# Kernel tuning notes

Hardware: AMD Instinct MI355X
Metric: run time of the kernel (lower is better)

## Reference

```python
import jax, jax.numpy as jnp
import numpy as np

N_NODES = 100000
N_EDGES = 1600000
D_IN = 128
D_HID = 128
SCALE = 1.8
EPS = 1e-12


def setup_inputs() -> dict:
    key = jax.random.key(0)
    ks = jax.random.split(key, 7)
    x = jax.random.normal(ks[0], (N_NODES, D_IN), dtype=jnp.float32)
    W1 = jax.random.normal(ks[1], (D_HID, D_IN), dtype=jnp.float32) * 0.05
    b1 = jax.random.normal(ks[2], (D_HID,), dtype=jnp.float32) * 0.05
    W2 = jax.random.normal(ks[3], (D_HID, D_HID), dtype=jnp.float32) * 0.05
    b2 = jax.random.normal(ks[4], (D_HID,), dtype=jnp.float32) * 0.05
    src = jax.random.randint(ks[5], (N_EDGES,), 0, N_NODES, dtype=jnp.int64 if jax.config.jax_enable_x64 else jnp.int32)
    dst = jax.random.randint(ks[6], (N_EDGES,), 0, N_NODES, dtype=jnp.int64 if jax.config.jax_enable_x64 else jnp.int32)
    return {"x": x, "W1": W1, "b1": b1, "W2": W2, "b2": b2, "src": src, "dst": dst}


def reference(x, W1, b1, W2, b2, src, dst):
    N = x.shape[0]
    ones = jnp.ones((src.shape[0],), dtype=x.dtype)
    # GraphConv norm='both' degree normalizers (clamped to >=1 as in DGL)
    deg_out = jnp.maximum(jnp.zeros((N,), x.dtype).at[src].add(ones), 1.0)
    deg_in = jnp.maximum(jnp.zeros((N,), x.dtype).at[dst].add(ones), 1.0)
    norm_out = jax.lax.rsqrt(deg_out)[:, None]  # [N,1]
    norm_in = jax.lax.rsqrt(deg_in)[:, None]    # [N,1]

    def layer(h, W, b):
        # torch.nn.Linear: h @ W.T + b
        h = jnp.einsum('nd,kd->nk', h, W) + b
        # F.normalize(h, dim=1) * 1.8
        nrm = jnp.sqrt(jnp.sum(h * h, axis=1, keepdims=True))
        h = h / jnp.maximum(nrm, EPS) * SCALE
        # GraphConv (weight=False, bias=False, norm='both'):
        # D_out^{-1/2} -> sparse aggregate -> D_in^{-1/2}
        h = h * norm_out
        agg = jax.ops.segment_sum(h[src], dst, num_segments=N)
        return agg * norm_in

    h = layer(x, W1, b1)
    h = layer(h, W2, b2)
    return h
```

## Files before the change

### kernel.cpp

```cpp
#include <hip/hip_runtime.h>
#include <cstdint>
#include <cstddef>

#define D 128
#define NSCALE 1.8f
#define NEPS 1e-12f
#define EPB 2048
#define NBPAD 784
#define NLO 512
#define SCAP 9216
#define SRCB 23
#define SRCM 0x7FFFFF

typedef __attribute__((ext_vector_type(8))) short bf16x8;
typedef __attribute__((ext_vector_type(4))) float f32x4;

__device__ __forceinline__ ushort bf16_rtn(float f) {
    uint32_t u = __float_as_uint(f);
    u = u + 0x7FFFu + ((u >> 16) & 1u);
    return (ushort)(u >> 16);
}

__device__ __forceinline__ float blo(uint32_t u) { return __uint_as_float(u << 16); }
__device__ __forceinline__ float bhi(uint32_t u) { return __uint_as_float(u & 0xFFFF0000u); }

__global__ __launch_bounds__(256) void hist_high_kernel(const int* __restrict__ src,
                                                        const int* __restrict__ dst,
                                                        int* __restrict__ Hd,
                                                        int* __restrict__ Hs, int ne) {
    __shared__ int hd[256], hs[256];
    int t = threadIdx.x, b = blockIdx.x;
    hd[t] = 0; hs[t] = 0;
    __syncthreads();
    int base = b * EPB, end = min(ne, base + EPB);
    for (int i = base + t; i < end; i += 256) {
        atomicAdd(&hd[dst[i] >> 9], 1);
        atomicAdd(&hs[src[i] >> 9], 1);
    }
    __syncthreads();
    Hd[t * NBPAD + b] = hd[t];
    Hs[t * NBPAD + b] = hs[t];
}

__global__ __launch_bounds__(256) void scan_cols_kernel(int* __restrict__ Hd,
                                                        int* __restrict__ Hs,
                                                        int* __restrict__ total_d,
                                                        int* __restrict__ total_s, int nbk) {
    __shared__ int s[256];
    int* H = blockIdx.y ? Hs : Hd;
    int* tot = blockIdx.y ? total_s : total_d;
    int v = blockIdx.x, t = threadIdx.x;
    int base = v * NBPAD + 4 * t;
    int a0 = (4 * t + 0 < nbk) ? H[base + 0] : 0;
    int a1 = (4 * t + 1 < nbk) ? H[base + 1] : 0;
    int a2 = (4 * t + 2 < nbk) ? H[base + 2] : 0;
    int a3 = (4 * t + 3 < nbk) ? H[base + 3] : 0;
    int sum = a0 + a1 + a2 + a3;
    s[t] = sum;
    __syncthreads();
    #pragma unroll
    for (int off = 1; off < 256; off <<= 1) {
        int u = (t >= off) ? s[t - off] : 0;
        __syncthreads();
        s[t] += u;
        __syncthreads();
    }
    int excl = s[t] - sum;
    if (4 * t + 0 < nbk) H[base + 0] = excl;
    if (4 * t + 1 < nbk) H[base + 1] = excl + a0;
    if (4 * t + 2 < nbk) H[base + 2] = excl + a0 + a1;
    if (4 * t + 3 < nbk) H[base + 3] = excl + a0 + a1 + a2;
    if (t == 255) tot[v] = s[255];
}

__global__ __launch_bounds__(256) void scan_tot_kernel(const int* __restrict__ total_d,
                                                       const int* __restrict__ total_s,
                                                       int* __restrict__ Bd,
                                                       int* __restrict__ Bs, int hb) {
    __shared__ int s[256];
    const int* tot = blockIdx.x ? total_s : total_d;
    int* B = blockIdx.x ? Bs : Bd;
    int t = threadIdx.x;
    int val = (t < hb) ? tot[t] : 0;
    s[t] = val;
    __syncthreads();
    #pragma unroll
    for (int off = 1; off < 256; off <<= 1) {
        int u = (t >= off) ? s[t - off] : 0;
        __syncthreads();
        s[t] += u;
        __syncthreads();
    }
    if (t <= hb) B[t] = s[t] - val;
}

__global__ __launch_bounds__(256) void scatter_high_kernel(const int* __restrict__ src,
                                                           const int* __restrict__ dst,
                                                           const int* __restrict__ Hd,
                                                           const int* __restrict__ Hs,
                                                           const int* __restrict__ Bd,
                                                           const int* __restrict__ Bs,
                                                           uint32_t* __restrict__ spack,
                                                           ushort* __restrict__ ss_low,
                                                           int ne, int hb) {
    __shared__ int cur[256];
    int t = threadIdx.x, b = blockIdx.x;
    int base = b * EPB, end = min(ne, base + EPB);
    if (blockIdx.y == 0) {
        if (t < hb) cur[t] = Bd[t] + Hd[t * NBPAD + b];
        __syncthreads();
        for (int i = base + t; i < end; i += 256) {
            int d = dst[i], s = src[i];
            int pd = atomicAdd(&cur[d >> 9], 1);
            spack[pd] = ((uint32_t)(d & (NLO - 1)) << SRCB) | (uint32_t)s;
        }
    } else {
        if (t < hb) cur[t] = Bs[t] + Hs[t * NBPAD + b];
        __syncthreads();
        for (int i = base + t; i < end; i += 256) {
            int s = src[i];
            int ps = atomicAdd(&cur[s >> 9], 1);
            ss_low[ps] = (ushort)(s & (NLO - 1));
        }
    }
}

__global__ __launch_bounds__(1024) void bucket_sorthist_kernel(const uint32_t* __restrict__ spack,
                                                               const int* __restrict__ Bd,
                                                               const ushort* __restrict__ ss_low,
                                                               const int* __restrict__ Bs,
                                                               int* __restrict__ offs,
                                                               int* __restrict__ cnt_dst,
                                                               float* __restrict__ norm_in,
                                                               float* __restrict__ norm_out,
                                                               int* __restrict__ ssrc, int N) {
    __shared__ int h[NLO], sc[NLO], cur[NLO];
    __shared__ int inA[SCAP];
    __shared__ int stage[SCAP];
    int t = threadIdx.x, v = blockIdx.x;

    if (blockIdx.y == 1) {
        int beg = Bs[v], end = Bs[v + 1];
        if (t < NLO) h[t] = 0;
        __syncthreads();
        for (int i = beg + t; i < end; i += 1024) atomicAdd(&h[(int)ss_low[i]], 1);
        __syncthreads();
        int g = (v << 9) + t;
        if (t < NLO && g < N) norm_out[g] = rsqrtf((float)max(h[t], 1));
        return;
    }

    int beg = Bd[v], end = Bd[v + 1];
    int m = end - beg;
    bool staged = (m <= SCAP);

    if (t < NLO) h[t] = 0;
    if (staged) {
        __syncthreads();
        for (int i = beg + t; i < end; i += 1024) inA[i - beg] = (int)spack[i];
        __syncthreads();
        for (int i = t; i < m; i += 1024) atomicAdd(&h[((uint32_t)inA[i]) >> SRCB], 1);
    } else {
        __syncthreads();
        for (int i = beg + t; i < end; i += 1024) atomicAdd(&h[spack[i] >> SRCB], 1);
    }
    __syncthreads();
    int cnt = 0;
    if (t < NLO) { cnt = h[t]; sc[t] = cnt; }
    __syncthreads();
    #pragma unroll
    for (int off = 1; off < NLO; off <<= 1) {
        int u = (t >= off && t < NLO) ? sc[t - off] : 0;
        __syncthreads();
        if (t < NLO) sc[t] += u;
        __syncthreads();
    }
    int excl = (t < NLO) ? (sc[t] - cnt) : 0;
    int g = (v << 9) + t;
    if (t < NLO && g < N) {
        offs[g] = beg + excl;
        cnt_dst[g] = cnt;
        norm_in[g] = rsqrtf((float)max(cnt, 1));
    }
    if (staged) {
        if (t < NLO) cur[t] = excl;
        __syncthreads();
        for (int i = t; i < m; i += 1024) {
            uint32_t p = (uint32_t)inA[i];
            int pos = atomicAdd(&cur[p >> SRCB], 1);
            stage[pos] = (int)(p & SRCM);
        }
        __syncthreads();
        for (int j = t; j < m; j += 1024) ssrc[beg + j] = stage[j];
    } else {
        if (t < NLO) cur[t] = beg + excl;
        __syncthreads();
        for (int i = beg + t; i < end; i += 1024) {
            uint32_t p = spack[i];
            int pos = atomicAdd(&cur[p >> SRCB], 1);
            ssrc[pos] = (int)(p & SRCM);
        }
    }
}

__global__ __launch_bounds__(256, 2) void mlp_fused_kernel(const float* __restrict__ X,
                                                           const float* __restrict__ W1,
                                                           const float* __restrict__ b1,
                                                           const float* __restrict__ W2,
                                                           const float* __restrict__ post,
                                                           ushort* __restrict__ Q,
                                                           ushort* __restrict__ Abuf, int N) {
    __shared__ ushort Wf1[128 * 128];
    __shared__ ushort Wf2[128 * 128];

    const int t = threadIdx.x;
    const int wave = t >> 6;
    const int lane = t & 63;
    const int q = lane >> 4;
    const int l16 = lane & 15;

    if (blockIdx.x == 0 && t < 32) {
        if (t < 16) ((uint4*)(Q    + (size_t)N * D))[t]      = make_uint4(0u, 0u, 0u, 0u);
        else        ((uint4*)(Abuf + (size_t)N * D))[t - 16] = make_uint4(0u, 0u, 0u, 0u);
    }

    #pragma unroll
    for (int it = 0; it < 8; ++it) {
        int f = t + 256 * it;
        int j = f >> 8;
        int p = (f >> 6) & 3;
        int ln = f & 63;
        int m = ln & 15;
        int k0 = 32 * p + 8 * (ln >> 4);
        {
            int row = 32 * (j >> 1) + 8 * (m >> 2) + 4 * (j & 1) + (m & 3);
            const float* srcp = W1 + row * D + k0;
            float4 a0 = *(const float4*)(srcp);
            float4 a1 = *(const float4*)(srcp + 4);
            bf16x8 v;
            v[0] = (short)bf16_rtn(a0.x); v[1] = (short)bf16_rtn(a0.y);
            v[2] = (short)bf16_rtn(a0.z); v[3] = (short)bf16_rtn(a0.w);
            v[4] = (short)bf16_rtn(a1.x); v[5] = (short)bf16_rtn(a1.y);
            v[6] = (short)bf16_rtn(a1.z); v[7] = (short)bf16_rtn(a1.w);
            ((bf16x8*)Wf1)[f] = v;
        }
        {
            int row = 16 * j + m;
            const float* srcp = W2 + row * D + k0;
            float4 a0 = *(const float4*)(srcp);
            float4 a1 = *(const float4*)(srcp + 4);
            bf16x8 v;
            v[0] = (short)bf16_rtn(a0.x); v[1] = (short)bf16_rtn(a0.y);
            v[2] = (short)bf16_rtn(a0.z); v[3] = (short)bf16_rtn(a0.w);
            v[4] = (short)bf16_rtn(a1.x); v[5] = (short)bf16_rtn(a1.y);
            v[6] = (short)bf16_rtn(a1.z); v[7] = (short)bf16_rtn(a1.w);
            ((bf16x8*)Wf2)[f] = v;
        }
    }

    const int r0 = blockIdx.x * 128 + wave * 32;
    bf16x8 xhi[2][4], xlo[2][4];
    #pragma unroll
    for (int rt = 0; rt < 2; ++rt) {
        int row = r0 + rt * 16 + l16;
        bool ok = (row < N);
        const float* xr = X + (size_t)(ok ? row : 0) * D;
        #pragma unroll
        for (int p = 0; p < 4; ++p) {
            int k0 = 32 * p + 8 * q;
            float4 a0 = ok ? *(const float4*)(xr + k0)     : make_float4(0, 0, 0, 0);
            float4 a1 = ok ? *(const float4*)(xr + k0 + 4) : make_float4(0, 0, 0, 0);
            float fv[8] = {a0.x, a0.y, a0.z, a0.w, a1.x, a1.y, a1.z, a1.w};
            bf16x8 h, l;
            #pragma unroll
            for (int e = 0; e < 8; ++e) {
                uint32_t u = __float_as_uint(fv[e]);
                h[e] = (short)(u >> 16);
                float hf = __uint_as_float(u & 0xFFFF0000u);
                l[e] = (short)(__float_as_uint(fv[e] - hf) >> 16);
            }
            xhi[rt][p] = h;
            xlo[rt][p] = l;
        }
    }

    __syncthreads();

    f32x4 acc1[2][8];
    #pragma unroll
    for (int rt = 0; rt < 2; ++rt)
        #pragma unroll
        for (int j = 0; j < 8; ++j) acc1[rt][j] = (f32x4){0.f, 0.f, 0.f, 0.f};

    #pragma unroll
    for (int p = 0; p < 4; ++p) {
        #pragma unroll
        for (int j = 0; j < 8; ++j) {
            bf16x8 wf = ((bf16x8*)Wf1)[(j * 4 + p) * 64 + lane];
            acc1[0][j] = __builtin_amdgcn_mfma_f32_16x16x32_bf16(wf, xhi[0][p], acc1[0][j], 0, 0, 0);
            acc1[0][j] = __builtin_amdgcn_mfma_f32_16x16x32_bf16(wf, xlo[0][p], acc1[0][j], 0, 0, 0);
            acc1[1][j] = __builtin_amdgcn_mfma_f32_16x16x32_bf16(wf, xhi[1][p], acc1[1][j], 0, 0, 0);
            acc1[1][j] = __builtin_amdgcn_mfma_f32_16x16x32_bf16(wf, xlo[1][p], acc1[1][j], 0, 0, 0);
        }
    }

    #pragma unroll
    for (int rt = 0; rt < 2; ++rt) {
        int node = r0 + rt * 16 + l16;
        float po = (node < N) ? post[node] : 0.f;
        float ss = 0.f;
        #pragma unroll
        for (int j = 0; j < 8; ++j) {
            const float4 bq = *(const float4*)(b1 + 32 * (j >> 1) + 8 * q + 4 * (j & 1));
            float v0 = acc1[rt][j][0] + bq.x; acc1[rt][j][0] = v0; ss += v0 * v0;
            float v1 = acc1[rt][j][1] + bq.y; acc1[rt][j][1] = v1; ss += v1 * v1;
            float v2 = acc1[rt][j][2] + bq.z; acc1[rt][j][2] = v2; ss += v2 * v2;
            float v3 = acc1[rt][j][3] + bq.w; acc1[rt][j][3] = v3; ss += v3 * v3;
        }
        ss += __shfl_xor(ss, 16);
        ss += __shfl_xor(ss, 32);
        float fsc = NSCALE / fmaxf(sqrtf(ss), NEPS) * po;
        #pragma unroll
        for (int j = 0; j < 8; ++j) {
            acc1[rt][j][0] *= fsc; acc1[rt][j][1] *= fsc;
            acc1[rt][j][2] *= fsc; acc1[rt][j][3] *= fsc;
        }
    }

    f32x4 acc2[2][8];
    #pragma unroll
    for (int rt = 0; rt < 2; ++rt)
        #pragma unroll
        for (int j = 0; j < 8; ++j) acc2[rt][j] = (f32x4){0.f, 0.f, 0.f, 0.f};

    #pragma unroll
    for (int p = 0; p < 4; ++p) {
        bf16x8 p2h0, p2l0, p2h1, p2l1;
        #pragma unroll
        for (int e = 0; e < 8; ++e) {
            float v0 = acc1[0][2 * p + (e >> 2)][e & 3];
            uint32_t u0 = __float_as_uint(v0);
            p2h0[e] = (short)(u0 >> 16);
            p2l0[e] = (short)(__float_as_uint(v0 - __uint_as_float(u0 & 0xFFFF0000u)) >> 16);
            float v1 = acc1[1][2 * p + (e >> 2)][e & 3];
            uint32_t u1 = __float_as_uint(v1);
            p2h1[e] = (short)(u1 >> 16);
            p2l1[e] = (short)(__float_as_uint(v1 - __uint_as_float(u1 & 0xFFFF0000u)) >> 16);
        }
        #pragma unroll
        for (int j = 0; j < 8; ++j) {
            bf16x8 wf = ((bf16x8*)Wf2)[(j * 4 + p) * 64 + lane];
            acc2[0][j] = __builtin_amdgcn_mfma_f32_16x16x32_bf16(wf, p2h0, acc2[0][j], 0, 0, 0);
            acc2[0][j] = __builtin_amdgcn_mfma_f32_16x16x32_bf16(wf, p2l0, acc2[0][j], 0, 0, 0);
            acc2[1][j] = __builtin_amdgcn_mfma_f32_16x16x32_bf16(wf, p2h1, acc2[1][j], 0, 0, 0);
            acc2[1][j] = __builtin_amdgcn_mfma_f32_16x16x32_bf16(wf, p2l1, acc2[1][j], 0, 0, 0);
        }
    }

    #pragma unroll
    for (int rt = 0; rt < 2; ++rt) {
        int node = r0 + rt * 16 + l16;
        if (node < N) {
            ushort* qp = Q + (size_t)node * D + 4 * q;
            #pragma unroll
            for (int j = 0; j < 8; ++j) {
                ushort4 s4;
                s4.x = bf16_rtn(acc2[rt][j][0]);
                s4.y = bf16_rtn(acc2[rt][j][1]);
                s4.z = bf16_rtn(acc2[rt][j][2]);
                s4.w = bf16_rtn(acc2[rt][j][3]);
                *(ushort4*)(qp + 16 * j) = s4;
            }
        }
    }
}

__global__ __launch_bounds__(256) void agg_mid_kernel(const ushort* __restrict__ A,
                                                      const int* __restrict__ sorted_src,
                                                      const int* __restrict__ offs,
                                                      const int* __restrict__ cnt,
                                                      const float* __restrict__ norm_in,
                                                      const float* __restrict__ norm_out,
                                                      const float* __restrict__ b2,
                                                      ushort* __restrict__ Abuf, int N) {
    int wave = threadIdx.x >> 6;
    int n0 = (blockIdx.x * 4 + wave) * 2;
    if (n0 >= N) return;
    int lane = threadIdx.x & 63;
    int g = lane >> 4;
    int c = lane & 15;
    const ushort* Ac = A + c * 8;

    int n1 = n0 + 1;
    int beg0 = offs[n0], len0 = cnt[n0];
    int beg1 = 0, len1 = 0;
    if (n1 < N) { beg1 = offs[n1]; len1 = cnt[n1]; }
    int last0 = beg0 + len0 - 1;
    int last1 = beg1 + len1 - 1;

    float a0[8] = {0.f, 0.f, 0.f, 0.f, 0.f, 0.f, 0.f, 0.f};
    float a1[8] = {0.f, 0.f, 0.f, 0.f, 0.f, 0.f, 0.f, 0.f};

    int mx = max(len0, len1);
    for (int i = 0; i < mx; i += 16) {
        int idx[8];
        #pragma unroll
        for (int k = 0; k < 4; ++k) {
            int e = beg0 + i + g + 4 * k;
            int cl = max(min(e, last0), 0);
            idx[k] = sorted_src[cl];
            if (e > last0) idx[k] = N;
        }
        #pragma unroll
        for (int k = 0; k < 4; ++k) {
            int e = beg1 + i + g + 4 * k;
            int cl = max(min(e, last1), 0);
            idx[4 + k] = sorted_src[cl];
            if (e > last1) idx[4 + k] = N;
        }
        uint4 w[8];
        #pragma unroll
        for (int k = 0; k < 8; ++k) w[k] = *(const uint4*)(Ac + (size_t)idx[k] * D);
        #pragma unroll
        for (int k = 0; k < 4; ++k) {
            a0[0] += blo(w[k].x); a0[1] += bhi(w[k].x);
            a0[2] += blo(w[k].y); a0[3] += bhi(w[k].y);
            a0[4] += blo(w[k].z); a0[5] += bhi(w[k].z);
            a0[6] += blo(w[k].w); a0[7] += bhi(w[k].w);
        }
        #pragma unroll
        for (int k = 4; k < 8; ++k) {
            a1[0] += blo(w[k].x); a1[1] += bhi(w[k].x);
            a1[2] += blo(w[k].y); a1[3] += bhi(w[k].y);
            a1[4] += blo(w[k].z); a1[5] += bhi(w[k].z);
            a1[6] += blo(w[k].w); a1[7] += bhi(w[k].w);
        }
    }

    #pragma unroll
    for (int e = 0; e < 8; ++e) {
        a0[e] += __shfl_xor(a0[e], 16);
        a0[e] += __shfl_xor(a0[e], 32);
        a1[e] += __shfl_xor(a1[e], 16);
        a1[e] += __shfl_xor(a1[e], 32);
    }

    float4 bql = *(const float4*)(b2 + c * 8);
    float4 bqh = *(const float4*)(b2 + c * 8 + 4);
    float bb[8] = {bql.x, bql.y, bql.z, bql.w, bqh.x, bqh.y, bqh.z, bqh.w};

    {
        float ni = norm_in[n0];
        float y[8];
        float ss = 0.f;
        #pragma unroll
        for (int e = 0; e < 8; ++e) { y[e] = a0[e] * ni + bb[e]; ss += y[e] * y[e]; }
        ss += __shfl_xor(ss, 1); ss += __shfl_xor(ss, 2);
        ss += __shfl_xor(ss, 4); ss += __shfl_xor(ss, 8);
        float fsc = NSCALE / fmaxf(sqrtf(ss), NEPS) * norm_out[n0];
        if (g == 0) {
            ushort4 s0, s1;
            s0.x = bf16_rtn(y[0] * fsc); s0.y = bf16_rtn(y[1] * fsc);
            s0.z = bf16_rtn(y[2] * fsc); s0.w = bf16_rtn(y[3] * fsc);
            s1.x = bf16_rtn(y[4] * fsc); s1.y = bf16_rtn(y[5] * fsc);
            s1.z = bf16_rtn(y[6] * fsc); s1.w = bf16_rtn(y[7] * fsc);
            ushort* op = Abuf + (size_t)n0 * D + c * 8;
            *(ushort4*)(op) = s0;
            *(ushort4*)(op + 4) = s1;
        }
    }
    if (n1 < N) {
        float ni = norm_in[n1];
        float y[8];
        float ss = 0.f;
        #pragma unroll
        for (int e = 0; e < 8; ++e) { y[e] = a1[e] * ni + bb[e]; ss += y[e] * y[e]; }
        ss += __shfl_xor(ss, 1); ss += __shfl_xor(ss, 2);
        ss += __shfl_xor(ss, 4); ss += __shfl_xor(ss, 8);
        float fsc = NSCALE / fmaxf(sqrtf(ss), NEPS) * norm_out[n1];
        if (g == 0) {
            ushort4 s0, s1;
            s0.x = bf16_rtn(y[0] * fsc); s0.y = bf16_rtn(y[1] * fsc);
            s0.z = bf16_rtn(y[2] * fsc); s0.w = bf16_rtn(y[3] * fsc);
            s1.x = bf16_rtn(y[4] * fsc); s1.y = bf16_rtn(y[5] * fsc);
            s1.z = bf16_rtn(y[6] * fsc); s1.w = bf16_rtn(y[7] * fsc);
            ushort* op = Abuf + (size_t)n1 * D + c * 8;
            *(ushort4*)(op) = s0;
            *(ushort4*)(op + 4) = s1;
        }
    }
}

__global__ __launch_bounds__(256) void agg_kernel(const ushort* __restrict__ A,
                                                  const int* __restrict__ sorted_src,
                                                  const int* __restrict__ offs,
                                                  const int* __restrict__ cnt,
                                                  const float* __restrict__ norm_in,
                                                  float* __restrict__ out, int N) {
    int wave = threadIdx.x >> 6;
    int n0 = (blockIdx.x * 4 + wave) * 2;
    if (n0 >= N) return;
    int lane = threadIdx.x & 63;
    int g = lane >> 4;
    int c = lane & 15;
    const ushort* Ac = A + c * 8;

    int n1 = n0 + 1;
    int beg0 = offs[n0], len0 = cnt[n0];
    int beg1 = 0, len1 = 0;
    if (n1 < N) { beg1 = offs[n1]; len1 = cnt[n1]; }
    int last0 = beg0 + len0 - 1;
    int last1 = beg1 + len1 - 1;

    float a0[8] = {0.f, 0.f, 0.f, 0.f, 0.f, 0.f, 0.f, 0.f};
    float a1[8] = {0.f, 0.f, 0.f, 0.f, 0.f, 0.f, 0.f, 0.f};

    int mx = max(len0, len1);
    for (int i = 0; i < mx; i += 16) {
        int idx[8];
        #pragma unroll
        for (int k = 0; k < 4; ++k) {
            int e = beg0 + i + g + 4 * k;
            int cl = max(min(e, last0), 0);
            idx[k] = sorted_src[cl];
            if (e > last0) idx[k] = N;
        }
        #pragma unroll
        for (int k = 0; k < 4; ++k) {
            int e = beg1 + i + g + 4 * k;
            int cl = max(min(e, last1), 0);
            idx[4 + k] = sorted_src[cl];
            if (e > last1) idx[4 + k] = N;
        }
        uint4 w[8];
        #pragma unroll
        for (int k = 0; k < 8; ++k) w[k] = *(const uint4*)(Ac + (size_t)idx[k] * D);
        #pragma unroll
        for (int k = 0; k < 4; ++k) {
            a0[0] += blo(w[k].x); a0[1] += bhi(w[k].x);
            a0[2] += blo(w[k].y); a0[3] += bhi(w[k].y);
            a0[4] += blo(w[k].z); a0[5] += bhi(w[k].z);
            a0[6] += blo(w[k].w); a0[7] += bhi(w[k].w);
        }
        #pragma unroll
        for (int k = 4; k < 8; ++k) {
            a1[0] += blo(w[k].x); a1[1] += bhi(w[k].x);
            a1[2] += blo(w[k].y); a1[3] += bhi(w[k].y);
            a1[4] += blo(w[k].z); a1[5] += bhi(w[k].z);
            a1[6] += blo(w[k].w); a1[7] += bhi(w[k].w);
        }
    }

    #pragma unroll
    for (int e = 0; e < 8; ++e) {
        a0[e] += __shfl_xor(a0[e], 16);
        a0[e] += __shfl_xor(a0[e], 32);
        a1[e] += __shfl_xor(a1[e], 16);
        a1[e] += __shfl_xor(a1[e], 32);
    }

    if (g == 0) {
        float sc0 = norm_in[n0];
        float* op0 = out + (size_t)n0 * D + c * 8;
        *(float4*)(op0)     = make_float4(a0[0] * sc0, a0[1] * sc0, a0[2] * sc0, a0[3] * sc0);
        *(float4*)(op0 + 4) = make_float4(a0[4] * sc0, a0[5] * sc0, a0[6] * sc0, a0[7] * sc0);
        if (n1 < N) {
            float sc1 = norm_in[n1];
            float* op1 = out + (size_t)n1 * D + c * 8;
            *(float4*)(op1)     = make_float4(a1[0] * sc1, a1[1] * sc1, a1[2] * sc1, a1[3] * sc1);
            *(float4*)(op1 + 4) = make_float4(a1[4] * sc1, a1[5] * sc1, a1[6] * sc1, a1[7] * sc1);
        }
    }
}


extern "C" void kernel_launch(void* const* d_in, const int* in_sizes, int n_in,
                              void* d_out, int out_size, void* d_ws, size_t ws_size,
                              hipStream_t stream) {
    const float* x  = (const float*)d_in[0];
    const float* W1 = (const float*)d_in[1];
    const float* b1 = (const float*)d_in[2];
    const float* W2 = (const float*)d_in[3];
    const float* b2 = (const float*)d_in[4];
    const int* src  = (const int*)d_in[5];
    const int* dst  = (const int*)d_in[6];
    float* out = (float*)d_out;

    const int N  = in_sizes[0] / D;
    const int NE = in_sizes[5];
    const int NBK = (NE + EPB - 1) / EPB;
    const int HB  = (N + NLO - 1) / NLO;

    char* w = (char*)d_ws;
    auto take = [&](size_t bytes) { char* p = w; w += (bytes + 255) & ~(size_t)255; return p; };
    int*      Hd       = (int*)take((size_t)256 * NBPAD * 4);
    int*      Hs       = (int*)take((size_t)256 * NBPAD * 4);
    int*      total_d  = (int*)take(256 * 4);
    int*      total_s  = (int*)take(256 * 4);
    int*      Bd       = (int*)take((size_t)(HB + 1) * 4);
    int*      Bs       = (int*)take((size_t)(HB + 1) * 4);
    uint32_t* spack    = (uint32_t*)take((size_t)NE * 4);
    ushort*   ss_low   = (ushort*)take((size_t)NE * 2);
    int*      ssrc     = (int*)take((size_t)NE * 4);
    int*      offs     = (int*)take((size_t)N * 4);
    int*      cnt_dst  = (int*)take((size_t)N * 4);
    float*    norm_in  = (float*)take((size_t)N * 4);
    float*    norm_out = (float*)take((size_t)N * 4);
    ushort*   Qbuf     = (ushort*)take((size_t)(N + 1) * D * 2);
    ushort*   Abuf     = (ushort*)take((size_t)(N + 1) * D * 2);

    hist_high_kernel<<<NBK, 256, 0, stream>>>(src, dst, Hd, Hs, NE);
    scan_cols_kernel<<<dim3(HB, 2), 256, 0, stream>>>(Hd, Hs, total_d, total_s, NBK);
    scan_tot_kernel<<<2, 256, 0, stream>>>(total_d, total_s, Bd, Bs, HB);
    scatter_high_kernel<<<dim3(NBK, 2), 256, 0, stream>>>(src, dst, Hd, Hs, Bd, Bs,
                                                          spack, ss_low, NE, HB);
    bucket_sorthist_kernel<<<dim3(HB, 2), 1024, 0, stream>>>(spack, Bd, ss_low, Bs,
                                                             offs, cnt_dst, norm_in,
                                                             norm_out, ssrc, N);

    const int mlp_blocks = (N + 127) / 128;
    const int agg_blocks = (N + 7) / 8;

    mlp_fused_kernel<<<mlp_blocks, 256, 0, stream>>>(x, W1, b1, W2, norm_out, Qbuf, Abuf, N);
    agg_mid_kernel<<<agg_blocks, 256, 0, stream>>>(Qbuf, ssrc, offs, cnt_dst,
                                                   norm_in, norm_out, b2, Abuf, N);
    agg_kernel<<<agg_blocks, 256, 0, stream>>>(Abuf, ssrc, offs, cnt_dst, norm_in, out, N);
}
```

Measured before the change: 306.6 us.

## Locally sort edges in shared memory before scattering to coarse buckets

The high-digit scatter now does a block-local counting sort in shared memory, so global writes to spack and ss_low land in contiguous per-bucket runs instead of being scattered one at a time. The dst and src passes share one block that reads each edge once, and the edges-per-block count doubles to 4096 with 512 threads. The histogram layout changes to block-major, so scan_cols now reads it with a stride. This costs extra shared-memory passes, more barriers and more LDS use per block, which lowers occupancy.

```diff
diff --git a/kernel.cpp b/kernel.cpp
--- a/kernel.cpp
+++ b/kernel.cpp
@@ -5,8 +5,7 @@
 #define D 128
 #define NSCALE 1.8f
 #define NEPS 1e-12f
-#define EPB 2048
-#define NBPAD 784
+#define EPB 4096
 #define NLO 512
 #define SCAP 9216
 #define SRCB 23
@@ -24,22 +23,24 @@
 __device__ __forceinline__ float blo(uint32_t u) { return __uint_as_float(u << 16); }
 __device__ __forceinline__ float bhi(uint32_t u) { return __uint_as_float(u & 0xFFFF0000u); }
 
-__global__ __launch_bounds__(256) void hist_high_kernel(const int* __restrict__ src,
+__global__ __launch_bounds__(512) void hist_high_kernel(const int* __restrict__ src,
                                                         const int* __restrict__ dst,
                                                         int* __restrict__ Hd,
                                                         int* __restrict__ Hs, int ne) {
     __shared__ int hd[256], hs[256];
     int t = threadIdx.x, b = blockIdx.x;
-    hd[t] = 0; hs[t] = 0;
+    if (t < 256) { hd[t] = 0; hs[t] = 0; }
     __syncthreads();
     int base = b * EPB, end = min(ne, base + EPB);
-    for (int i = base + t; i < end; i += 256) {
+    for (int i = base + t; i < end; i += 512) {
         atomicAdd(&hd[dst[i] >> 9], 1);
         atomicAdd(&hs[src[i] >> 9], 1);
     }
     __syncthreads();
-    Hd[t * NBPAD + b] = hd[t];
-    Hs[t * NBPAD + b] = hs[t];
+    if (t < 256) {
+        Hd[b * 256 + t] = hd[t];
+        Hs[b * 256 + t] = hs[t];
+    }
 }
 
 __global__ __launch_bounds__(256) void scan_cols_kernel(int* __restrict__ Hd,
@@ -50,11 +51,10 @@
     int* H = blockIdx.y ? Hs : Hd;
     int* tot = blockIdx.y ? total_s : total_d;
     int v = blockIdx.x, t = threadIdx.x;
-    int base = v * NBPAD + 4 * t;
-    int a0 = (4 * t + 0 < nbk) ? H[base + 0] : 0;
-    int a1 = (4 * t + 1 < nbk) ? H[base + 1] : 0;
-    int a2 = (4 * t + 2 < nbk) ? H[base + 2] : 0;
-    int a3 = (4 * t + 3 < nbk) ? H[base + 3] : 0;
+    int a0 = (4 * t + 0 < nbk) ? H[(4 * t + 0) * 256 + v] : 0;
+    int a1 = (4 * t + 1 < nbk) ? H[(4 * t + 1) * 256 + v] : 0;
+    int a2 = (4 * t + 2 < nbk) ? H[(4 * t + 2) * 256 + v] : 0;
+    int a3 = (4 * t + 3 < nbk) ? H[(4 * t + 3) * 256 + v] : 0;
     int sum = a0 + a1 + a2 + a3;
     s[t] = sum;
     __syncthreads();
@@ -66,10 +66,10 @@
         __syncthreads();
     }
     int excl = s[t] - sum;
-    if (4 * t + 0 < nbk) H[base + 0] = excl;
-    if (4 * t + 1 < nbk) H[base + 1] = excl + a0;
-    if (4 * t + 2 < nbk) H[base + 2] = excl + a0 + a1;
-    if (4 * t + 3 < nbk) H[base + 3] = excl + a0 + a1 + a2;
+    if (4 * t + 0 < nbk) H[(4 * t + 0) * 256 + v] = excl;
+    if (4 * t + 1 < nbk) H[(4 * t + 1) * 256 + v] = excl + a0;
+    if (4 * t + 2 < nbk) H[(4 * t + 2) * 256 + v] = excl + a0 + a1;
+    if (4 * t + 3 < nbk) H[(4 * t + 3) * 256 + v] = excl + a0 + a1 + a2;
     if (t == 255) tot[v] = s[255];
 }
 
@@ -94,7 +94,7 @@
     if (t <= hb) B[t] = s[t] - val;
 }
 
-__global__ __launch_bounds__(256) void scatter_high_kernel(const int* __restrict__ src,
+__global__ __launch_bounds__(512) void scatter_sort_kernel(const int* __restrict__ src,
                                                            const int* __restrict__ dst,
                                                            const int* __restrict__ Hd,
                                                            const int* __restrict__ Hs,
@@ -103,26 +103,88 @@
                                                            uint32_t* __restrict__ spack,
                                                            ushort* __restrict__ ss_low,
                                                            int ne, int hb) {
-    __shared__ int cur[256];
+    __shared__ int hist[256], sc[256], cur[256], gbase[256];
+    __shared__ uint32_t sbuf[EPB];
+    __shared__ uint8_t binb[EPB];
     int t = threadIdx.x, b = blockIdx.x;
-    int base = b * EPB, end = min(ne, base + EPB);
-    if (blockIdx.y == 0) {
-        if (t < hb) cur[t] = Bd[t] + Hd[t * NBPAD + b];
-        __syncthreads();
-        for (int i = base + t; i < end; i += 256) {
-            int d = dst[i], s = src[i];
-            int pd = atomicAdd(&cur[d >> 9], 1);
-            spack[pd] = ((uint32_t)(d & (NLO - 1)) << SRCB) | (uint32_t)s;
-        }
-    } else {
-        if (t < hb) cur[t] = Bs[t] + Hs[t * NBPAD + b];
-        __syncthreads();
-        for (int i = base + t; i < end; i += 256) {
-            int s = src[i];
-            int ps = atomicAdd(&cur[s >> 9], 1);
-            ss_low[ps] = (ushort)(s & (NLO - 1));
-        }
-    }
+    int base = b * EPB, end = min(ne, base + EPB), m = end - base;
+
+    int myd[8], mys[8];
+    #pragma unroll
+    for (int k = 0; k < 8; ++k) {
+        int i = base + t + 512 * k;
+        bool ok = (i < end);
+        myd[k] = ok ? dst[i] : -1;
+        mys[k] = ok ? src[i] : -1;
+    }
+
+    if (t < 256) hist[t] = 0;
+    __syncthreads();
+    #pragma unroll
+    for (int k = 0; k < 8; ++k)
+        if (myd[k] >= 0) atomicAdd(&hist[myd[k] >> 9], 1);
+    __syncthreads();
+    if (t < 256) sc[t] = hist[t];
+    __syncthreads();
+    #pragma unroll
+    for (int off = 1; off < 256; off <<= 1) {
+        int u = (t >= off && t < 256) ? sc[t - off] : 0;
+        __syncthreads();
+        if (t < 256) sc[t] += u;
+        __syncthreads();
+    }
+    if (t < 256) {
+        int excl = sc[t] - hist[t];
+        cur[t] = excl;
+        if (t < hb) gbase[t] = Bd[t] + Hd[b * 256 + t] - excl;
+    }
+    __syncthreads();
+    #pragma unroll
+    for (int k = 0; k < 8; ++k) {
+        if (myd[k] >= 0) {
+            int bin = myd[k] >> 9;
+            int pos = atomicAdd(&cur[bin], 1);
+            sbuf[pos] = ((uint32_t)(myd[k] & (NLO - 1)) << SRCB) | (uint32_t)mys[k];
+            binb[pos] = (uint8_t)bin;
+        }
+    }
+    __syncthreads();
+    for (int i = t; i < m; i += 512) spack[gbase[binb[i]] + i] = sbuf[i];
+    __syncthreads();
+
+    if (t < 256) hist[t] = 0;
+    __syncthreads();
+    #pragma unroll
+    for (int k = 0; k < 8; ++k)
+        if (mys[k] >= 0) atomicAdd(&hist[mys[k] >> 9], 1);
+    __syncthreads();
+    if (t < 256) sc[t] = hist[t];
+    __syncthreads();
+    #pragma unroll
+    for (int off = 1; off < 256; off <<= 1) {
+        int u = (t >= off && t < 256) ? sc[t - off] : 0;
+        __syncthreads();
+        if (t < 256) sc[t] += u;
+        __syncthreads();
+    }
+    if (t < 256) {
+        int excl = sc[t] - hist[t];
+        cur[t] = excl;
+        if (t < hb) gbase[t] = Bs[t] + Hs[b * 256 + t] - excl;
+    }
+    __syncthreads();
+    ushort* sb2 = (ushort*)sbuf;
+    #pragma unroll
+    for (int k = 0; k < 8; ++k) {
+        if (mys[k] >= 0) {
+            int bin = mys[k] >> 9;
+            int pos = atomicAdd(&cur[bin], 1);
+            sb2[pos] = (ushort)(mys[k] & (NLO - 1));
+            binb[pos] = (uint8_t)bin;
+        }
+    }
+    __syncthreads();
+    for (int i = t; i < m; i += 512) ss_low[gbase[binb[i]] + i] = sb2[i];
 }
 
 __global__ __launch_bounds__(1024) void bucket_sorthist_kernel(const uint32_t* __restrict__ spack,
@@ -593,8 +655,8 @@
 
     char* w = (char*)d_ws;
     auto take = [&](size_t bytes) { char* p = w; w += (bytes + 255) & ~(size_t)255; return p; };
-    int*      Hd       = (int*)take((size_t)256 * NBPAD * 4);
-    int*      Hs       = (int*)take((size_t)256 * NBPAD * 4);
+    int*      Hd       = (int*)take((size_t)NBK * 256 * 4);
+    int*      Hs       = (int*)take((size_t)NBK * 256 * 4);
     int*      total_d  = (int*)take(256 * 4);
     int*      total_s  = (int*)take(256 * 4);
     int*      Bd       = (int*)take((size_t)(HB + 1) * 4);
@@ -609,11 +671,11 @@
     ushort*   Qbuf     = (ushort*)take((size_t)(N + 1) * D * 2);
     ushort*   Abuf     = (ushort*)take((size_t)(N + 1) * D * 2);
 
-    hist_high_kernel<<<NBK, 256, 0, stream>>>(src, dst, Hd, Hs, NE);
+    hist_high_kernel<<<NBK, 512, 0, stream>>>(src, dst, Hd, Hs, NE);
     scan_cols_kernel<<<dim3(HB, 2), 256, 0, stream>>>(Hd, Hs, total_d, total_s, NBK);
     scan_tot_kernel<<<2, 256, 0, stream>>>(total_d, total_s, Bd, Bs, HB);
-    scatter_high_kernel<<<dim3(NBK, 2), 256, 0, stream>>>(src, dst, Hd, Hs, Bd, Bs,
-                                                          spack, ss_low, NE, HB);
+    scatter_sort_kernel<<<NBK, 512, 0, stream>>>(src, dst, Hd, Hs, Bd, Bs,
+                                                 spack, ss_low, NE, HB);
     bucket_sorthist_kernel<<<dim3(HB, 2), 1024, 0, stream>>>(spack, Bd, ss_low, Bs,
                                                              offs, cnt_dst, norm_in,
                                                              norm_out, ssrc, N);
```

New measurement: 298.3 us. 1.03x faster.
